# Performance work log

Measured on AMD Instinct MI355X. Metric: run time of the kernel, lower is better.

Reference implementation:

```python
import jax, jax.numpy as jnp
import numpy as np

NUM_CODES = 512
CODE_DIM = 64
COMMITMENT_COST = 0.25


def setup_inputs() -> dict:
    key = jax.random.key(0)
    k1, k2 = jax.random.split(key)
    latents = jax.random.normal(k1, (32, 4096, CODE_DIM), dtype=jnp.float32)
    # nn.Embedding weight init: uniform(-1/num_codes, 1/num_codes)
    codebook = jax.random.uniform(
        k2, (NUM_CODES, CODE_DIM), dtype=jnp.float32,
        minval=-1.0 / NUM_CODES, maxval=1.0 / NUM_CODES)
    return {"latents": latents, "codebook": codebook}


def reference(latents, codebook):
    shape = latents.shape
    flat = latents.reshape(-1, CODE_DIM)                      # [N, D]
    x2 = jnp.sum(flat * flat, axis=-1, keepdims=True)         # [N, 1]
    c2 = jnp.sum(codebook * codebook, axis=-1)                # [K]
    xc = flat @ codebook.T                                    # [N, K] dense GEMM
    dist2 = x2 - 2.0 * xc + c2[None, :]
    codes = jnp.argmin(dist2, axis=-1)                        # [N] int
    quantized = codebook[codes].reshape(shape)                # gather + reshape
    sg = jax.lax.stop_gradient
    commitment_loss = jnp.mean((latents - sg(quantized)) ** 2)
    embedding_loss = jnp.mean((quantized - sg(latents)) ** 2)
    vq_loss = embedding_loss + COMMITMENT_COST * commitment_loss
    quantized_st = latents + sg(quantized - latents)          # straight-through
    return quantized_st, codes.reshape(shape[:-1]), vq_loss
```

## Files before the change

### kernel.cpp

```cpp
#include <hip/hip_runtime.h>

#define NUM_CODES 512
#define CODE_DIM 64
#define N_ROWS (32 * 4096)
#define ROWS_PER_BLOCK 64
#define WAVES_PER_BLOCK 4
#define CODES_PER_WAVE (NUM_CODES / WAVES_PER_BLOCK)

typedef float f32x16 __attribute__((ext_vector_type(16)));

static __device__ inline const float* uniform_ptr(const float* p) {
    uint64_t u = (uint64_t)p;
    uint32_t lo = __builtin_amdgcn_readfirstlane((uint32_t)u);
    uint32_t hi = __builtin_amdgcn_readfirstlane((uint32_t)(u >> 32));
    return (const float*)(((uint64_t)hi << 32) | lo);
}

__global__ void vq_precompute_c2(const float* __restrict__ cb,
                                 float* __restrict__ c2) {
    int k = blockIdx.x * blockDim.x + threadIdx.x;
    if (k < NUM_CODES) {
        const float* c = cb + (size_t)k * CODE_DIM;
        float s = 0.f;
#pragma unroll
        for (int d = 0; d < CODE_DIM; ++d) s = fmaf(c[d], c[d], s);
        c2[k] = s;
    }
}

__global__ __launch_bounds__(256, 4) void vq_main(
    const float* __restrict__ latents, const float* __restrict__ cb,
    const float* __restrict__ c2g, float* __restrict__ out_q,
    float* __restrict__ out_codes, float* __restrict__ loss_accum) {
    const int lane = threadIdx.x & 63;
    const int wave = threadIdx.x >> 6;
    const int row = blockIdx.x * ROWS_PER_BLOCK + lane;
    const int chunk0 = wave * CODES_PER_WAVE;

    const float* __restrict__ x = latents + (size_t)row * CODE_DIM;
    float xv[CODE_DIM];
#pragma unroll
    for (int i = 0; i < CODE_DIM / 4; ++i) {
        float4 v = reinterpret_cast<const float4*>(x)[i];
        xv[4 * i + 0] = v.x;
        xv[4 * i + 1] = v.y;
        xv[4 * i + 2] = v.z;
        xv[4 * i + 3] = v.w;
    }
    float x2 = 0.f;
#pragma unroll
    for (int d = 0; d < CODE_DIM; ++d) x2 = fmaf(xv[d], xv[d], x2);

    float bestd = __builtin_inff();
    int bk = 0;
    const float* cp = uniform_ptr(cb + (size_t)chunk0 * CODE_DIM);
    const float* zp = uniform_ptr(c2g + chunk0);

#pragma unroll 1
    for (int k = 0; k < CODES_PER_WAVE; ++k) {
        f32x16 c0, c1, c2, c3;
        float zz;
        asm volatile("s_load_dwordx16 %0, %1, 0x00" : "=s"(c0) : "s"(cp));
        asm volatile("s_load_dwordx16 %0, %1, 0x40" : "=s"(c1) : "s"(cp));
        asm volatile("s_load_dwordx16 %0, %1, 0x80" : "=s"(c2) : "s"(cp));
        asm volatile("s_load_dwordx16 %0, %1, 0xc0" : "=s"(c3) : "s"(cp));
        asm volatile("s_load_dword %0, %1, 0x00" : "=s"(zz) : "s"(zp));
        asm volatile("s_waitcnt lgkmcnt(0)"
                     : "+s"(c0), "+s"(c1), "+s"(c2), "+s"(c3), "+s"(zz));

        float s = 0.f;
#pragma unroll
        for (int q = 0; q < 16; ++q) s = fmaf(xv[q], c0[q], s);
#pragma unroll
        for (int q = 0; q < 16; ++q) s = fmaf(xv[16 + q], c1[q], s);
#pragma unroll
        for (int q = 0; q < 16; ++q) s = fmaf(xv[32 + q], c2[q], s);
#pragma unroll
        for (int q = 0; q < 16; ++q) s = fmaf(xv[48 + q], c3[q], s);

        float dist = (x2 - 2.0f * s) + zz;
        if (dist < bestd) { bestd = dist; bk = chunk0 + k; }
        cp += CODE_DIM;
        zp += 1;
    }

    __shared__ float sdist[WAVES_PER_BLOCK][ROWS_PER_BLOCK];
    __shared__ int sidx[WAVES_PER_BLOCK][ROWS_PER_BLOCK];
    __shared__ int sbi[ROWS_PER_BLOCK];
    sdist[wave][lane] = bestd;
    sidx[wave][lane] = bk;
    __syncthreads();
    if (wave == 0) {
        float bd = sdist[0][lane];
        int bi = sidx[0][lane];
#pragma unroll
        for (int w = 1; w < WAVES_PER_BLOCK; ++w) {
            float d = sdist[w][lane];
            int i = sidx[w][lane];
            if (d < bd) { bd = d; bi = i; }
        }
        sbi[lane] = bi;
    }
    __syncthreads();

    float lsum = 0.f;
#pragma unroll
    for (int rr = 0; rr < 16; ++rr) {
        const int r = wave * 16 + rr;
        const size_t grow = (size_t)blockIdx.x * ROWS_PER_BLOCK + r;
        const int bi = sbi[r];
        float xd = latents[grow * CODE_DIM + lane];
        float qd = cb[(size_t)bi * CODE_DIM + lane];
        float e = xd - qd;
        lsum = fmaf(e, e, lsum);
        out_q[grow * CODE_DIM + lane] = xd + (qd - xd);
        if (lane == 0) out_codes[grow] = (float)bi;
    }
#pragma unroll
    for (int off = 32; off > 0; off >>= 1) lsum += __shfl_down(lsum, off);
    __shared__ float red[WAVES_PER_BLOCK];
    if (lane == 0) red[wave] = lsum;
    __syncthreads();
    if (threadIdx.x == 0)
        atomicAdd(loss_accum, red[0] + red[1] + red[2] + red[3]);
}

__global__ void vq_finalize(const float* __restrict__ acc,
                            float* __restrict__ out_loss) {
    *out_loss = 1.25f * (*acc) / (float)(N_ROWS * CODE_DIM);
}

extern "C" void kernel_launch(void* const* d_in, const int* in_sizes, int n_in,
                              void* d_out, int out_size, void* d_ws, size_t ws_size,
                              hipStream_t stream) {
    const float* latents = (const float*)d_in[0];
    const float* cb      = (const float*)d_in[1];

    float* out_q     = (float*)d_out;
    float* out_codes = out_q + (size_t)N_ROWS * CODE_DIM;
    float* out_loss  = out_codes + N_ROWS;

    float* c2  = (float*)d_ws;
    float* acc = c2 + NUM_CODES;

    hipMemsetAsync(acc, 0, sizeof(float), stream);
    vq_precompute_c2<<<2, 256, 0, stream>>>(cb, c2);
    vq_main<<<N_ROWS / ROWS_PER_BLOCK, 256, 0, stream>>>(latents, cb, c2, out_q,
                                                         out_codes, acc);
    vq_finalize<<<1, 1, 0, stream>>>(acc, out_loss);
}
```

Measured before the change: 227.5 us.

## Replace per-row scalar codebook loop with LDS-staged 8x8 register-tiled distance GEMM

The distance computation becomes a register-blocked outer product. Each block handles 32 rows, which are transposed into LDS. The codebook is staged into LDS in 8-dim chunks, and each thread accumulates an 8-row by 8-code tile. The argmin is then finished with wave shuffles, breaking ties toward the lower index. This removes the per-code scalar-load wait latency of the old one-row-per-lane loop, and each LDS vector read now feeds many FMAs. In exchange, every block re-reads the full codebook from cache, the kernel adds barriers per chunk, and the transposed LDS stores may cause bank conflicts.

```diff
diff --git a/kernel.cpp b/kernel.cpp
--- a/kernel.cpp
+++ b/kernel.cpp
@@ -3,112 +3,125 @@
 #define NUM_CODES 512
 #define CODE_DIM 64
 #define N_ROWS (32 * 4096)
-#define ROWS_PER_BLOCK 64
-#define WAVES_PER_BLOCK 4
-#define CODES_PER_WAVE (NUM_CODES / WAVES_PER_BLOCK)
+#define RPB 32
+#define DC 8
+#define NCHUNK (CODE_DIM / DC)
+#define CBLK 12
 
-typedef float f32x16 __attribute__((ext_vector_type(16)));
-
-static __device__ inline const float* uniform_ptr(const float* p) {
-    uint64_t u = (uint64_t)p;
-    uint32_t lo = __builtin_amdgcn_readfirstlane((uint32_t)u);
-    uint32_t hi = __builtin_amdgcn_readfirstlane((uint32_t)(u >> 32));
-    return (const float*)(((uint64_t)hi << 32) | lo);
-}
-
-__global__ void vq_precompute_c2(const float* __restrict__ cb,
-                                 float* __restrict__ c2) {
-    int k = blockIdx.x * blockDim.x + threadIdx.x;
-    if (k < NUM_CODES) {
-        const float* c = cb + (size_t)k * CODE_DIM;
-        float s = 0.f;
+__global__ void vq_prep(const float* __restrict__ cb, float* __restrict__ c2) {
+    int k = blockIdx.x * 64 + threadIdx.x;
+    const float* c = cb + (size_t)k * CODE_DIM;
+    float s = 0.f;
 #pragma unroll
-        for (int d = 0; d < CODE_DIM; ++d) s = fmaf(c[d], c[d], s);
-        c2[k] = s;
-    }
+    for (int d = 0; d < CODE_DIM; ++d) s = fmaf(c[d], c[d], s);
+    c2[k] = s;
 }
 
 __global__ __launch_bounds__(256, 4) void vq_main(
     const float* __restrict__ latents, const float* __restrict__ cb,
     const float* __restrict__ c2g, float* __restrict__ out_q,
     float* __restrict__ out_codes, float* __restrict__ loss_accum) {
-    const int lane = threadIdx.x & 63;
-    const int wave = threadIdx.x >> 6;
-    const int row = blockIdx.x * ROWS_PER_BLOCK + lane;
-    const int chunk0 = wave * CODES_PER_WAVE;
+    const int tid = threadIdx.x;
+    const int lane = tid & 63;
+    const int wave = tid >> 6;
+    const size_t R0 = (size_t)blockIdx.x * RPB;
 
-    const float* __restrict__ x = latents + (size_t)row * CODE_DIM;
-    float xv[CODE_DIM];
+    __shared__ float xT[CODE_DIM][RPB];
+    __shared__ float cT[DC][64][CBLK];
+    __shared__ float c2s[NUM_CODES];
+    __shared__ float x2s[RPB];
+    __shared__ int sbi[RPB];
+    __shared__ float red[4];
+
+    {
+        int r = tid >> 3;
+        int d0 = (tid & 7) * 8;
+        const float* xp = latents + (R0 + r) * CODE_DIM + d0;
+        float4 a = *(const float4*)(xp);
+        float4 b = *(const float4*)(xp + 4);
+        xT[d0 + 0][r] = a.x; xT[d0 + 1][r] = a.y;
+        xT[d0 + 2][r] = a.z; xT[d0 + 3][r] = a.w;
+        xT[d0 + 4][r] = b.x; xT[d0 + 5][r] = b.y;
+        xT[d0 + 6][r] = b.z; xT[d0 + 7][r] = b.w;
+    }
+    if (tid < NUM_CODES / 4)
+        ((float4*)c2s)[tid] = ((const float4*)c2g)[tid];
+    __syncthreads();
+
+    if (lane < 8) {
+        int r = wave * 8 + lane;
+        float s = 0.f;
 #pragma unroll
-    for (int i = 0; i < CODE_DIM / 4; ++i) {
-        float4 v = reinterpret_cast<const float4*>(x)[i];
-        xv[4 * i + 0] = v.x;
-        xv[4 * i + 1] = v.y;
-        xv[4 * i + 2] = v.z;
-        xv[4 * i + 3] = v.w;
+        for (int d = 0; d < CODE_DIM; ++d) s = fmaf(xT[d][r], xT[d][r], s);
+        x2s[r] = s;
     }
-    float x2 = 0.f;
+
+    float acc[8][8];
 #pragma unroll
-    for (int d = 0; d < CODE_DIM; ++d) x2 = fmaf(xv[d], xv[d], x2);
-
-    float bestd = __builtin_inff();
-    int bk = 0;
-    const float* cp = uniform_ptr(cb + (size_t)chunk0 * CODE_DIM);
-    const float* zp = uniform_ptr(c2g + chunk0);
+    for (int r = 0; r < 8; ++r)
+#pragma unroll
+        for (int k = 0; k < 8; ++k) acc[r][k] = 0.f;
 
 #pragma unroll 1
-    for (int k = 0; k < CODES_PER_WAVE; ++k) {
-        f32x16 c0, c1, c2, c3;
-        float zz;
-        asm volatile("s_load_dwordx16 %0, %1, 0x00" : "=s"(c0) : "s"(cp));
-        asm volatile("s_load_dwordx16 %0, %1, 0x40" : "=s"(c1) : "s"(cp));
-        asm volatile("s_load_dwordx16 %0, %1, 0x80" : "=s"(c2) : "s"(cp));
-        asm volatile("s_load_dwordx16 %0, %1, 0xc0" : "=s"(c3) : "s"(cp));
-        asm volatile("s_load_dword %0, %1, 0x00" : "=s"(zz) : "s"(zp));
-        asm volatile("s_waitcnt lgkmcnt(0)"
-                     : "+s"(c0), "+s"(c1), "+s"(c2), "+s"(c3), "+s"(zz));
-
-        float s = 0.f;
+    for (int ch = 0; ch < NCHUNK; ++ch) {
 #pragma unroll
-        for (int q = 0; q < 16; ++q) s = fmaf(xv[q], c0[q], s);
+        for (int p = 0; p < 2; ++p) {
+            int c = p * 256 + tid;
+            const float* gp = cb + (size_t)c * CODE_DIM + ch * DC;
+            float4 a = *(const float4*)(gp);
+            float4 b = *(const float4*)(gp + 4);
+            int blk = c >> 3, e = c & 7;
+            cT[0][blk][e] = a.x; cT[1][blk][e] = a.y;
+            cT[2][blk][e] = a.z; cT[3][blk][e] = a.w;
+            cT[4][blk][e] = b.x; cT[5][blk][e] = b.y;
+            cT[6][blk][e] = b.z; cT[7][blk][e] = b.w;
+        }
+        __syncthreads();
 #pragma unroll
-        for (int q = 0; q < 16; ++q) s = fmaf(xv[16 + q], c1[q], s);
+        for (int dl = 0; dl < DC; ++dl) {
+            float xf[8], cf[8];
+            *(float4*)&xf[0] = *(const float4*)&xT[ch * DC + dl][wave * 8];
+            *(float4*)&xf[4] = *(const float4*)&xT[ch * DC + dl][wave * 8 + 4];
+            *(float4*)&cf[0] = *(const float4*)&cT[dl][lane][0];
+            *(float4*)&cf[4] = *(const float4*)&cT[dl][lane][4];
 #pragma unroll
-        for (int q = 0; q < 16; ++q) s = fmaf(xv[32 + q], c2[q], s);
+            for (int r = 0; r < 8; ++r)
 #pragma unroll
-        for (int q = 0; q < 16; ++q) s = fmaf(xv[48 + q], c3[q], s);
-
-        float dist = (x2 - 2.0f * s) + zz;
-        if (dist < bestd) { bestd = dist; bk = chunk0 + k; }
-        cp += CODE_DIM;
-        zp += 1;
+                for (int k = 0; k < 8; ++k)
+                    acc[r][k] = fmaf(xf[r], cf[k], acc[r][k]);
+        }
+        __syncthreads();
     }
 
-    __shared__ float sdist[WAVES_PER_BLOCK][ROWS_PER_BLOCK];
-    __shared__ int sidx[WAVES_PER_BLOCK][ROWS_PER_BLOCK];
-    __shared__ int sbi[ROWS_PER_BLOCK];
-    sdist[wave][lane] = bestd;
-    sidx[wave][lane] = bk;
-    __syncthreads();
-    if (wave == 0) {
-        float bd = sdist[0][lane];
-        int bi = sidx[0][lane];
+    float c2f[8];
+    *(float4*)&c2f[0] = *(const float4*)&c2s[lane * 8];
+    *(float4*)&c2f[4] = *(const float4*)&c2s[lane * 8 + 4];
 #pragma unroll
-        for (int w = 1; w < WAVES_PER_BLOCK; ++w) {
-            float d = sdist[w][lane];
-            int i = sidx[w][lane];
-            if (d < bd) { bd = d; bi = i; }
+    for (int r = 0; r < 8; ++r) {
+        float x2v = x2s[wave * 8 + r];
+        float bd = __builtin_inff();
+        int bk = 0;
+#pragma unroll
+        for (int k = 0; k < 8; ++k) {
+            float dist = (x2v - 2.0f * acc[r][k]) + c2f[k];
+            if (dist < bd) { bd = dist; bk = lane * 8 + k; }
         }
-        sbi[lane] = bi;
+#pragma unroll
+        for (int off = 32; off > 0; off >>= 1) {
+            float od = __shfl_down(bd, off);
+            int oi = __shfl_down(bk, off);
+            if (od < bd || (od == bd && oi < bk)) { bd = od; bk = oi; }
+        }
+        if (lane == 0) sbi[wave * 8 + r] = bk;
     }
     __syncthreads();
 
     float lsum = 0.f;
 #pragma unroll
-    for (int rr = 0; rr < 16; ++rr) {
-        const int r = wave * 16 + rr;
-        const size_t grow = (size_t)blockIdx.x * ROWS_PER_BLOCK + r;
-        const int bi = sbi[r];
+    for (int rr = 0; rr < 8; ++rr) {
+        int r = wave * 8 + rr;
+        size_t grow = R0 + r;
+        int bi = sbi[r];
         float xd = latents[grow * CODE_DIM + lane];
         float qd = cb[(size_t)bi * CODE_DIM + lane];
         float e = xd - qd;
@@ -118,11 +131,9 @@
     }
 #pragma unroll
     for (int off = 32; off > 0; off >>= 1) lsum += __shfl_down(lsum, off);
-    __shared__ float red[WAVES_PER_BLOCK];
     if (lane == 0) red[wave] = lsum;
     __syncthreads();
-    if (threadIdx.x == 0)
-        atomicAdd(loss_accum, red[0] + red[1] + red[2] + red[3]);
+    if (tid == 0) atomicAdd(loss_accum, red[0] + red[1] + red[2] + red[3]);
 }
 
 __global__ void vq_finalize(const float* __restrict__ acc,
@@ -144,8 +155,8 @@
     float* acc = c2 + NUM_CODES;
 
     hipMemsetAsync(acc, 0, sizeof(float), stream);
-    vq_precompute_c2<<<2, 256, 0, stream>>>(cb, c2);
-    vq_main<<<N_ROWS / ROWS_PER_BLOCK, 256, 0, stream>>>(latents, cb, c2, out_q,
-                                                         out_codes, acc);
+    vq_prep<<<NUM_CODES / 64, 64, 0, stream>>>(cb, c2);
+    vq_main<<<N_ROWS / RPB, 256, 0, stream>>>(latents, cb, c2, out_q,
+                                              out_codes, acc);
     vq_finalize<<<1, 1, 0, stream>>>(acc, out_loss);
 }
```

After: 220.4 us. 3.1% less time.
